# Kernel optimization log

Hardware: AMD Instinct MI355X
Metric: run time of the kernel (lower is better)

## Reference

```python
import jax, jax.numpy as jnp
import numpy as np

EPS = 1e-8
NUM_ITER = 3
NUM_SLOTS = 8
NUM_HEADS = 4


def _ln(x, w, b):
    m = x.mean(-1, keepdims=True)
    v = x.var(-1, keepdims=True)
    return (x - m) / jnp.sqrt(v + 1e-5) * w + b


def setup_inputs() -> dict:
    key = jax.random.key(0)
    B, T, N, D, S, H = 16, 12, 1024, 256, 128, 256
    K = NUM_SLOTS
    ks = jax.random.split(key, 32)
    w = lambda i, shape: (0.02 * jax.random.normal(ks[i], shape)).astype(jnp.float32)
    f32 = jnp.float32
    return {
        'inputs': jax.random.normal(ks[0], (B, T, N, D), f32),
        'slots_noise': jax.random.normal(ks[1], (B, K, S), f32),
        'slot_mu': w(2, (1, 1, S)),
        'slot_log_sigma': w(3, (1, 1, S)),
        'ln_in_w': jnp.ones((D,), f32), 'ln_in_b': jnp.zeros((D,), f32),
        'ln_slots_w': jnp.ones((S,), f32), 'ln_slots_b': jnp.zeros((S,), f32),
        'ln_mlp_w': jnp.ones((S,), f32), 'ln_mlp_b': jnp.zeros((S,), f32),
        'Wq': w(4, (S, S)), 'Wk': w(5, (D, S)), 'Wv': w(6, (D, S)),
        'gru_Wih': w(7, (3 * S, S)), 'gru_Whh': w(8, (3 * S, S)),
        'gru_bih': jnp.zeros((3 * S,), f32), 'gru_bhh': jnp.zeros((3 * S,), f32),
        'mlp_W1': w(9, (S, H)), 'mlp_b1': jnp.zeros((H,), f32),
        'mlp_W2': w(10, (H, S)), 'mlp_b2': jnp.zeros((S,), f32),
        'p_ln1_w': jnp.ones((S,), f32), 'p_ln1_b': jnp.zeros((S,), f32),
        'p_Wq': w(11, (S, S)), 'p_Wk': w(12, (S, S)), 'p_Wv': w(13, (S, S)), 'p_Wo': w(14, (S, S)),
        'p_ln2_w': jnp.ones((S,), f32), 'p_ln2_b': jnp.zeros((S,), f32),
        'p_ffn_W1': w(15, (S, 4 * S)), 'p_ffn_b1': jnp.zeros((4 * S,), f32),
        'p_ffn_W2': w(16, (4 * S, S)), 'p_ffn_b2': jnp.zeros((S,), f32),
        'p_lnf_w': jnp.ones((S,), f32), 'p_lnf_b': jnp.zeros((S,), f32),
    }


def reference(inputs, slots_noise, slot_mu, slot_log_sigma,
              ln_in_w, ln_in_b, ln_slots_w, ln_slots_b, ln_mlp_w, ln_mlp_b,
              Wq, Wk, Wv, gru_Wih, gru_Whh, gru_bih, gru_bhh,
              mlp_W1, mlp_b1, mlp_W2, mlp_b2,
              p_ln1_w, p_ln1_b, p_Wq, p_Wk, p_Wv, p_Wo,
              p_ln2_w, p_ln2_b, p_ffn_W1, p_ffn_b1, p_ffn_W2, p_ffn_b2,
              p_lnf_w, p_lnf_b):
    B, T, N, D = inputs.shape
    S = slot_mu.shape[-1]
    K = NUM_SLOTS

    slots0 = slot_mu + jnp.exp(slot_log_sigma) * slots_noise  # (B,K,S)
    x = _ln(inputs, ln_in_w, ln_in_b)
    k = (x @ Wk) * (S ** -0.5)  # (B,T,N,S), pre-scaled keys
    v = x @ Wv                  # (B,T,N,S)

    def gru(u, h):  # torch GRUCell semantics; u,h: (B*K,S)
        gi = u @ gru_Wih.T + gru_bih
        gh = h @ gru_Whh.T + gru_bhh
        i_r, i_z, i_n = jnp.split(gi, 3, -1)
        h_r, h_z, h_n = jnp.split(gh, 3, -1)
        r = jax.nn.sigmoid(i_r + h_r)
        z = jax.nn.sigmoid(i_z + h_z)
        n = jnp.tanh(i_n + r * h_n)
        return (1.0 - z) * n + z * h

    def mha(y):  # (B,K,S) self-attention, pre-LN block style
        dh = S // NUM_HEADS
        split = lambda t: t.reshape(B, K, NUM_HEADS, dh).transpose(0, 2, 1, 3)
        q = split(y @ p_Wq) * (dh ** -0.5)
        kk = split(y @ p_Wk)
        vv = split(y @ p_Wv)
        a = jax.nn.softmax(jnp.einsum('bhqd,bhkd->bhqk', q, kk), -1)
        o = jnp.einsum('bhqk,bhkd->bhqd', a, vv).transpose(0, 2, 1, 3).reshape(B, K, S)
        return o @ p_Wo

    def predictor(s):
        s = s + mha(_ln(s, p_ln1_w, p_ln1_b))
        h = _ln(s, p_ln2_w, p_ln2_b)
        s = s + (jax.nn.relu(h @ p_ffn_W1 + p_ffn_b1) @ p_ffn_W2 + p_ffn_b2)
        return _ln(s, p_lnf_w, p_lnf_b)

    def step(slots, kv_t):
        k_t, v_t = kv_t  # (B,N,S) each
        attn_vis = None
        for i in range(NUM_ITER):
            slots_prev = slots
            q = _ln(slots, ln_slots_w, ln_slots_b) @ Wq          # (B,K,S)
            logits = jnp.einsum('bns,bks->bnk', k_t, q)           # (B,N,K)
            attn_vis = jax.nn.softmax(logits, -1)                 # over slots
            attn = attn_vis + EPS
            attn = attn / attn.sum(1, keepdims=True)              # normalize over inputs
            updates = jnp.einsum('bnk,bns->bks', attn, v_t)       # (B,K,S)
            slots = gru(updates.reshape(-1, S), slots_prev.reshape(-1, S)).reshape(B, K, S)
            if i < NUM_ITER - 1:
                h = _ln(slots, ln_mlp_w, ln_mlp_b)
                slots = slots + (jax.nn.relu(h @ mlp_W1 + mlp_b1) @ mlp_W2 + mlp_b2)
        return predictor(slots), (slots, attn_vis)

    kT = jnp.swapaxes(k, 0, 1)  # (T,B,N,S)
    vT = jnp.swapaxes(v, 0, 1)
    _, (slots_seq, attn_seq) = jax.lax.scan(step, slots0, (kT, vT))
    slots_collect = jnp.swapaxes(slots_seq, 0, 1)  # (B,T,K,S)
    attns_collect = jnp.swapaxes(attn_seq, 0, 1)   # (B,T,N,K)
    return slots_collect, attns_collect
```

## Files before the change

### kernel.cpp

```cpp
#include <hip/hip_runtime.h>
#include <hip/hip_bf16.h>

typedef _Float16 half8 __attribute__((ext_vector_type(8)));
typedef float floatx4 __attribute__((ext_vector_type(4)));

#define MFMA_F16(a, b, c) __builtin_amdgcn_mfma_f32_16x16x32_f16((a), (b), (c), 0, 0, 0)

struct PrepJobs {
  const float* src[13];
  _Float16* dst[13];
  int In[13], Out[13], elems[13], doT[13];
  float scale[13];
};

__global__ void prep_all_kernel(PrepJobs J) {
  int j = blockIdx.y;
  int idx = blockIdx.x * 256 + threadIdx.x;
  if (idx >= J.elems[j]) return;
  float v;
  if (J.doT[j]) { int o = idx / J.In[j], i = idx - o * J.In[j]; v = J.src[j][i * J.Out[j] + o]; }
  else          { v = J.src[j][idx]; }
  J.dst[j][idx] = (_Float16)(v * J.scale[j]);
}

__global__ void init_ctr_kernel(int* __restrict__ ctr) {
  if (threadIdx.x < 16) ctr[threadIdx.x] = 0;
}

__global__ __launch_bounds__(256) void gemm_kv_kernel(
    const float* __restrict__ x, const float* __restrict__ lnw_g,
    const float* __restrict__ lnb_g, const _Float16* __restrict__ WT,
    _Float16* __restrict__ kout, _Float16* __restrict__ vTout) {
  __shared__ union {
    struct { _Float16 A[128][72]; _Float16 B[128][72]; } s;
    _Float16 C[128][136];
  } u;
  __shared__ float s_mean[128], s_rstd[128], s_red[256][2], s_lnw[256], s_lnb[256];

  const int tid = threadIdx.x;
  const int bx = blockIdx.x, y = blockIdx.y;
  const size_t r0 = (size_t)bx * 128;
  const int w = tid >> 6, lane = tid & 63, quad = lane >> 4, l15 = lane & 15;

  s_lnw[tid] = lnw_g[tid];
  s_lnb[tid] = lnb_g[tid];
  {
    int row = tid >> 1, half = tid & 1;
    const float* p = x + (r0 + row) * 256 + half * 128;
    float s = 0.f, sq = 0.f;
    for (int i = 0; i < 32; i++) {
      float4 d = ((const float4*)p)[i];
      s += d.x + d.y + d.z + d.w;
      sq += d.x * d.x + d.y * d.y + d.z * d.z + d.w * d.w;
    }
    s_red[tid][0] = s; s_red[tid][1] = sq;
  }
  __syncthreads();
  if (tid < 128) {
    float s  = s_red[2 * tid][0] + s_red[2 * tid + 1][0];
    float sq = s_red[2 * tid][1] + s_red[2 * tid + 1][1];
    float m = s * (1.f / 256.f);
    float v = sq * (1.f / 256.f) - m * m;
    s_mean[tid] = m; s_rstd[tid] = rsqrtf(v + 1e-5f);
  }

  floatx4 acc[2][8];
  for (int rt = 0; rt < 2; rt++)
    for (int ct = 0; ct < 8; ct++) acc[rt][ct] = (floatx4){0.f, 0.f, 0.f, 0.f};

  for (int c = 0; c < 4; c++) {
    __syncthreads();
    for (int i = 0; i < 4; i++) {
      int g = tid + 256 * i;
      int row = g >> 3, c8 = g & 7;
      int col0 = c * 64 + c8 * 8;
      const float* p = x + (r0 + row) * 256 + col0;
      float4 d0 = ((const float4*)p)[0];
      float4 d1 = ((const float4*)p)[1];
      float f[8] = {d0.x, d0.y, d0.z, d0.w, d1.x, d1.y, d1.z, d1.w};
      float m = s_mean[row], rs = s_rstd[row];
      half8 hv;
      #pragma unroll
      for (int j = 0; j < 8; j++)
        hv[j] = (_Float16)((f[j] - m) * rs * s_lnw[col0 + j] + s_lnb[col0 + j]);
      *(half8*)&u.s.A[row][c8 * 8] = hv;
      *(half8*)&u.s.B[row][c8 * 8] = *(const half8*)(WT + (size_t)(y * 128 + row) * 256 + col0);
    }
    __syncthreads();
    #pragma unroll
    for (int ks = 0; ks < 2; ks++) {
      half8 af[2];
      af[0] = *(const half8*)&u.s.A[(2 * w) * 16 + l15][ks * 32 + quad * 8];
      af[1] = *(const half8*)&u.s.A[(2 * w + 1) * 16 + l15][ks * 32 + quad * 8];
      #pragma unroll
      for (int ct = 0; ct < 8; ct++) {
        half8 bf = *(const half8*)&u.s.B[ct * 16 + l15][ks * 32 + quad * 8];
        acc[0][ct] = MFMA_F16(af[0], bf, acc[0][ct]);
        acc[1][ct] = MFMA_F16(af[1], bf, acc[1][ct]);
      }
    }
  }

  const size_t bt = (size_t)(bx >> 3);
  const int n0loc = (bx & 7) * 128;
  if (y == 0) {
    for (int rt = 0; rt < 2; rt++)
      for (int ct = 0; ct < 8; ct++)
        #pragma unroll
        for (int r = 0; r < 4; r++) {
          size_t row = r0 + (2 * w + rt) * 16 + quad * 4 + r;
          kout[row * 128 + ct * 16 + l15] = (_Float16)acc[rt][ct][r];
        }
  } else {
    __syncthreads();
    for (int rt = 0; rt < 2; rt++)
      for (int ct = 0; ct < 8; ct++)
        #pragma unroll
        for (int r = 0; r < 4; r++)
          u.C[(2 * w + rt) * 16 + quad * 4 + r][ct * 16 + l15] = (_Float16)acc[rt][ct][r];
    __syncthreads();
    int s = tid >> 1, hf = tid & 1;
    for (int j = 0; j < 8; j++) {
      int nb = hf * 64 + j * 8;
      half8 tmp;
      #pragma unroll
      for (int e = 0; e < 8; e++) tmp[e] = u.C[nb + e][s];
      *(half8*)(vTout + (bt * 128 + s) * 1024 + n0loc + nb) = tmp;
    }
  }
}

struct P2Args {
  const _Float16 *kbuf, *vT;
  const _Float16 *WqT, *Wih, *Whh, *W1T, *W2T;
  const _Float16 *pQT, *pKT, *pVT, *pOT, *pF1T, *pF2T;
  const float *noise, *mu, *lsig;
  const float *lnsw, *lnsb, *lnmw, *lnmb;
  const float *bih, *bhh, *mb1, *mb2;
  const float *pl1w, *pl1b, *pl2w, *pl2b, *fb1, *fb2, *plfw, *plfb;
  float *out_slots, *out_attn;
  float *upd_p;
  float *col_p;
  float *vs_p;
  int   *ctr;
};

struct SH {
  _Float16 k_lds[128][136];
  _Float16 v_lds[128][136];
  float slots[8][128];
  _Float16 a16[16][136];
  _Float16 h16[16][136];
  float gi[8][384];
  float gh[8][384];
  union {
    struct { _Float16 qT[16][136]; _Float16 attnT[16][136]; } sa;
    struct { _Float16 m16[16][264]; } mlp;
    struct { float qh[8][128]; float kh[8][128]; float vh[8][128]; float sc[4][8][8]; } mha;
    struct { _Float16 f16[16][520]; } ffn;
  } u;
  float colsum[8];
  float vsum[128];
  float bih[384], bhh[384], mb1[256], mb2[128], fb1[512], fb2[128];
  float lnsw[128], lnsb[128], lnmw[128], lnmb[128];
  float pl1w[128], pl1b[128], pl2w[128], pl2b[128], plfw[128], plfb[128];
};

__device__ __forceinline__ void group_barrier(int* ctr, int target) {
  __syncthreads();
  if (threadIdx.x == 0) {
    __hip_atomic_fetch_add(ctr, 1, __ATOMIC_ACQ_REL, __HIP_MEMORY_SCOPE_AGENT);
    while (__hip_atomic_load(ctr, __ATOMIC_ACQUIRE, __HIP_MEMORY_SCOPE_AGENT) < target)
      __builtin_amdgcn_s_sleep(1);
  }
  __syncthreads();
}

__device__ __forceinline__ void ln_to_a16(SH* sh, const float (*src)[128],
                                          const float* wv, const float* bv,
                                          int w, int lane) {
  if (w < 8) {
    float x0 = src[w][lane], x1 = src[w][lane + 64];
    float s = x0 + x1, sq = x0 * x0 + x1 * x1;
    #pragma unroll
    for (int m = 1; m < 64; m <<= 1) { s += __shfl_xor(s, m); sq += __shfl_xor(sq, m); }
    float mn = s * 0.0078125f;
    float vr = sq * 0.0078125f - mn * mn;
    float rs = rsqrtf(vr + 1e-5f);
    sh->a16[w][lane]      = (_Float16)((x0 - mn) * rs * wv[lane]      + bv[lane]);
    sh->a16[w][lane + 64] = (_Float16)((x1 - mn) * rs * wv[lane + 64] + bv[lane + 64]);
  } else {
    sh->a16[w][lane] = (_Float16)0.f;
    sh->a16[w][lane + 64] = (_Float16)0.f;
  }
}

__global__ __launch_bounds__(1024, 4) void slot_attn_kernel(P2Args P) {
  __shared__ SH sh;
  const int tid = threadIdx.x;
  const int w = tid >> 6, lane = tid & 63, quad = lane >> 4, l15 = lane & 15;
  const int b = blockIdx.x & 15;
  const int g = blockIdx.x >> 4;
  const int n0 = g * 128;
  int* ctrb = P.ctr + b;
  int bar_phase = 0;

  for (int i = tid; i < 384; i += 1024) { sh.bih[i] = P.bih[i]; sh.bhh[i] = P.bhh[i]; }
  for (int i = tid; i < 256; i += 1024) sh.mb1[i] = P.mb1[i];
  for (int i = tid; i < 512; i += 1024) sh.fb1[i] = P.fb1[i];
  if (tid < 128) {
    sh.mb2[tid]  = P.mb2[tid];  sh.fb2[tid]  = P.fb2[tid];
    sh.lnsw[tid] = P.lnsw[tid]; sh.lnsb[tid] = P.lnsb[tid];
    sh.lnmw[tid] = P.lnmw[tid]; sh.lnmb[tid] = P.lnmb[tid];
    sh.pl1w[tid] = P.pl1w[tid]; sh.pl1b[tid] = P.pl1b[tid];
    sh.pl2w[tid] = P.pl2w[tid]; sh.pl2b[tid] = P.pl2b[tid];
    sh.plfw[tid] = P.plfw[tid]; sh.plfb[tid] = P.plfb[tid];
  }
  {
    int kk = tid >> 7, s = tid & 127;
    sh.slots[kk][s] = P.mu[s] + expf(P.lsig[s]) * P.noise[(b * 8 + kk) * 128 + s];
  }
  __syncthreads();

  for (int t = 0; t < 12; t++) {
    const _Float16* kt = P.kbuf + ((size_t)(b * 12 + t)) * 1024 * 128 + (size_t)n0 * 128;
    const _Float16* vt = P.vT   + ((size_t)(b * 12 + t)) * 128 * 1024 + n0;
    {
      int r = tid >> 4, c8 = (tid & 15) * 8;
      #pragma unroll
      for (int p = 0; p < 2; p++) {
        int row = p * 64 + r;
        *(half8*)&sh.k_lds[row][c8] = *(const half8*)(kt + (size_t)row * 128 + c8);
        *(half8*)&sh.v_lds[row][c8] = *(const half8*)(vt + (size_t)row * 1024 + c8);
      }
    }
    if (tid < 128) sh.vsum[tid] = 0.f;
    __syncthreads();
    {
      int s = tid >> 3, j = tid & 7;
      float a = 0.f;
      #pragma unroll
      for (int e = 0; e < 16; e++) a += (float)sh.v_lds[s][j * 16 + e];
      atomicAdd(&sh.vsum[s], a);
    }
    __syncthreads();
    if (tid < 128)
      __hip_atomic_store(&P.vs_p[(b * 8 + g) * 128 + tid], sh.vsum[tid],
                         __ATOMIC_RELAXED, __HIP_MEMORY_SCOPE_AGENT);

    for (int it = 0; it < 3; it++) {
      const int par = (t * 3 + it) & 1;
      float* updg = P.upd_p + ((size_t)(par * 16 + b) * 8 + g) * 1024;
      float* colg = P.col_p + ((size_t)(par * 16 + b) * 8 + g) * 8;
      if (w < 8) {
        float x0 = sh.slots[w][lane], x1 = sh.slots[w][lane + 64];
        sh.h16[w][lane] = (_Float16)x0; sh.h16[w][lane + 64] = (_Float16)x1;
        float s = x0 + x1, sq = x0 * x0 + x1 * x1;
        #pragma unroll
        for (int m = 1; m < 64; m <<= 1) { s += __shfl_xor(s, m); sq += __shfl_xor(sq, m); }
        float mn = s * 0.0078125f;
        float vr = sq * 0.0078125f - mn * mn;
        float rs = rsqrtf(vr + 1e-5f);
        sh.a16[w][lane]      = (_Float16)((x0 - mn) * rs * sh.lnsw[lane]      + sh.lnsb[lane]);
        sh.a16[w][lane + 64] = (_Float16)((x1 - mn) * rs * sh.lnsw[lane + 64] + sh.lnsb[lane + 64]);
      } else {
        sh.h16[w][lane] = (_Float16)0.f; sh.h16[w][lane + 64] = (_Float16)0.f;
        sh.a16[w][lane] = (_Float16)0.f; sh.a16[w][lane + 64] = (_Float16)0.f;
      }
      if (tid < 8) sh.colsum[tid] = 0.f;
      __syncthreads();
      if (w < 8) {
        floatx4 acc = (floatx4){0.f, 0.f, 0.f, 0.f};
        const _Float16* ar = &sh.a16[l15][quad * 8];
        const _Float16* br = P.WqT + (size_t)(w * 16 + l15) * 128 + quad * 8;
        #pragma unroll
        for (int ks = 0; ks < 4; ks++)
          acc = MFMA_F16(*(const half8*)(ar + ks * 32), *(const half8*)(br + ks * 32), acc);
        #pragma unroll
        for (int r = 0; r < 4; r++)
          sh.u.sa.qT[quad * 4 + r][w * 16 + l15] = (_Float16)acc[r];
      } else {
        const int idx8 = w - 8;
        const _Float16* ar = &sh.h16[l15][quad * 8];
        #pragma unroll
        for (int tt = 0; tt < 2; tt++) {
          int ct = idx8 + tt * 8;
          const _Float16* Bg = P.Whh + (size_t)(ct * 16 + l15) * 128 + quad * 8;
          floatx4 acc = (floatx4){0.f, 0.f, 0.f, 0.f};
          #pragma unroll
          for (int ks = 0; ks < 4; ks++)
            acc = MFMA_F16(*(const half8*)(ar + ks * 32), *(const half8*)(Bg + ks * 32), acc);
          int col = ct * 16 + l15;
          #pragma unroll
          for (int r = 0; r < 4; r++) {
            int slot = quad * 4 + r;
            if (slot < 8) sh.gh[slot][col] = acc[r] + sh.bhh[col];
          }
        }
      }
      __syncthreads();
      if (w < 8) {
        int nloc0 = w * 16;
        floatx4 acc = (floatx4){0.f, 0.f, 0.f, 0.f};
        const _Float16* ar = &sh.k_lds[nloc0 + l15][quad * 8];
        const _Float16* br = &sh.u.sa.qT[l15][quad * 8];
        #pragma unroll
        for (int ks = 0; ks < 4; ks++)
          acc = MFMA_F16(*(const half8*)(ar + ks * 32), *(const half8*)(br + ks * 32), acc);
        float cs = 0.f;
        #pragma unroll
        for (int r = 0; r < 4; r++) {
          float v = (l15 < 8) ? acc[r] : -3.0e38f;
          float mx = v;
          mx = fmaxf(mx, __shfl_xor(mx, 1, 16));
          mx = fmaxf(mx, __shfl_xor(mx, 2, 16));
          mx = fmaxf(mx, __shfl_xor(mx, 4, 16));
          mx = fmaxf(mx, __shfl_xor(mx, 8, 16));
          float pv = (l15 < 8) ? expf(v - mx) : 0.f;
          float ss = pv;
          ss += __shfl_xor(ss, 1, 16); ss += __shfl_xor(ss, 2, 16);
          ss += __shfl_xor(ss, 4, 16); ss += __shfl_xor(ss, 8, 16);
          float pn = pv / ss;
          cs += pn;
          int nloc = nloc0 + quad * 4 + r;
          sh.u.sa.attnT[l15][nloc] = (_Float16)pn;
          if (it == 2 && l15 < 8)
            P.out_attn[((size_t)(b * 12 + t) * 1024 + n0 + nloc) * 8 + l15] = pn;
        }
        cs += __shfl_xor(cs, 16); cs += __shfl_xor(cs, 32);
        if (lane < 8) atomicAdd(&sh.colsum[lane], cs);
      } else {
        const int idx8 = w - 8;
        int ct = idx8 + 16;
        const _Float16* ar = &sh.h16[l15][quad * 8];
        const _Float16* Bg = P.Whh + (size_t)(ct * 16 + l15) * 128 + quad * 8;
        floatx4 acc = (floatx4){0.f, 0.f, 0.f, 0.f};
        #pragma unroll
        for (int ks = 0; ks < 4; ks++)
          acc = MFMA_F16(*(const half8*)(ar + ks * 32), *(const half8*)(Bg + ks * 32), acc);
        int col = ct * 16 + l15;
        #pragma unroll
        for (int r = 0; r < 4; r++) {
          int slot = quad * 4 + r;
          if (slot < 8) sh.gh[slot][col] = acc[r] + sh.bhh[col];
        }
      }
      __syncthreads();
      if (w < 8) {
        floatx4 acc = (floatx4){0.f, 0.f, 0.f, 0.f};
        const _Float16* ar = &sh.u.sa.attnT[l15][quad * 8];
        const _Float16* br = &sh.v_lds[w * 16 + l15][quad * 8];
        #pragma unroll
        for (int ks = 0; ks < 4; ks++)
          acc = MFMA_F16(*(const half8*)(ar + ks * 32), *(const half8*)(br + ks * 32), acc);
        int scol = w * 16 + l15;
        #pragma unroll
        for (int r = 0; r < 4; r++) {
          int slot = quad * 4 + r;
          if (slot < 8)
            __hip_atomic_store(&updg[slot * 128 + scol], acc[r],
                               __ATOMIC_RELAXED, __HIP_MEMORY_SCOPE_AGENT);
        }
      }
      if (tid < 8)
        __hip_atomic_store(&colg[tid], sh.colsum[tid],
                           __ATOMIC_RELAXED, __HIP_MEMORY_SCOPE_AGENT);
      bar_phase++;
      group_barrier(ctrb, 8 * bar_phase);
      {
        int slot = tid >> 7, scol = tid & 127;
        const float* up = P.upd_p + (size_t)(par * 16 + b) * 8 * 1024 + slot * 128 + scol;
        float sum = 0.f;
        #pragma unroll
        for (int gg = 0; gg < 8; gg++)
          sum += __hip_atomic_load((float*)(up + gg * 1024),
                                   __ATOMIC_RELAXED, __HIP_MEMORY_SCOPE_AGENT);
        float csum = 0.f;
        if (tid < 8) {
          const float* cp = P.col_p + (size_t)(par * 16 + b) * 8 * 8 + tid;
          #pragma unroll
          for (int gg = 0; gg < 8; gg++)
            csum += __hip_atomic_load((float*)(cp + gg * 8),
                                      __ATOMIC_RELAXED, __HIP_MEMORY_SCOPE_AGENT);
        }
        float vtot = 0.f;
        if (it == 0 && tid < 128) {
          const float* vp = P.vs_p + b * 8 * 128 + tid;
          #pragma unroll
          for (int gg = 0; gg < 8; gg++)
            vtot += __hip_atomic_load((float*)(vp + gg * 128),
                                      __ATOMIC_RELAXED, __HIP_MEMORY_SCOPE_AGENT);
        }
        __syncthreads();
        if (tid < 8) sh.colsum[tid] = csum;
        if (it == 0 && tid < 128) sh.vsum[tid] = vtot;
        __syncthreads();
        float upd = (sum + 1e-8f * sh.vsum[scol]) / (sh.colsum[slot] + 1024.f * 1e-8f);
        sh.a16[slot][scol] = (_Float16)upd;
      }
      __syncthreads();
      {
        const _Float16* ar = &sh.a16[l15][quad * 8];
        const _Float16* Bg = P.Wih + (size_t)(w * 16 + l15) * 128 + quad * 8;
        floatx4 acc = (floatx4){0.f, 0.f, 0.f, 0.f};
        #pragma unroll
        for (int ks = 0; ks < 4; ks++)
          acc = MFMA_F16(*(const half8*)(ar + ks * 32), *(const half8*)(Bg + ks * 32), acc);
        int col = w * 16 + l15;
        #pragma unroll
        for (int r = 0; r < 4; r++) {
          int slot = quad * 4 + r;
          if (slot < 8) sh.gi[slot][col] = acc[r] + sh.bih[col];
        }
        if (w < 8) {
          int col2 = (16 + w) * 16 + l15;
          const _Float16* Bg2 = P.Wih + (size_t)((16 + w) * 16 + l15) * 128 + quad * 8;
          floatx4 acc2 = (floatx4){0.f, 0.f, 0.f, 0.f};
          #pragma unroll
          for (int ks = 0; ks < 4; ks++)
            acc2 = MFMA_F16(*(const half8*)(ar + ks * 32), *(const half8*)(Bg2 + ks * 32), acc2);
          #pragma unroll
          for (int r = 0; r < 4; r++) {
            int slot = quad * 4 + r;
            if (slot < 8) sh.gi[slot][col2] = acc2[r] + sh.bih[col2];
          }
        }
      }
      __syncthreads();
      if (w < 8) {
        float h0 = sh.slots[w][lane], h1 = sh.slots[w][lane + 64];
        float r0 = 1.f / (1.f + expf(-(sh.gi[w][lane]       + sh.gh[w][lane])));
        float z0 = 1.f / (1.f + expf(-(sh.gi[w][128 + lane] + sh.gh[w][128 + lane])));
        float n0v = tanhf(sh.gi[w][256 + lane] + r0 * sh.gh[w][256 + lane]);
        float x0 = (1.f - z0) * n0v + z0 * h0;
        int l64 = lane + 64;
        float r1 = 1.f / (1.f + expf(-(sh.gi[w][l64]       + sh.gh[w][l64])));
        float z1 = 1.f / (1.f + expf(-(sh.gi[w][128 + l64] + sh.gh[w][128 + l64])));
        float n1v = tanhf(sh.gi[w][256 + l64] + r1 * sh.gh[w][256 + l64]);
        float x1 = (1.f - z1) * n1v + z1 * h1;
        sh.slots[w][lane] = x0; sh.slots[w][lane + 64] = x1;
        if (it == 2 && g == 0) {
          P.out_slots[((size_t)(b * 12 + t) * 8 + w) * 128 + lane]      = x0;
          P.out_slots[((size_t)(b * 12 + t) * 8 + w) * 128 + lane + 64] = x1;
        }
        const float* wv = (it < 2) ? sh.lnmw : sh.pl1w;
        const float* bv = (it < 2) ? sh.lnmb : sh.pl1b;
        float s = x0 + x1, sq = x0 * x0 + x1 * x1;
        #pragma unroll
        for (int m = 1; m < 64; m <<= 1) { s += __shfl_xor(s, m); sq += __shfl_xor(sq, m); }
        float mn = s * 0.0078125f;
        float vr = sq * 0.0078125f - mn * mn;
        float rs = rsqrtf(vr + 1e-5f);
        sh.a16[w][lane]      = (_Float16)((x0 - mn) * rs * wv[lane]      + bv[lane]);
        sh.a16[w][lane + 64] = (_Float16)((x1 - mn) * rs * wv[lane + 64] + bv[lane + 64]);
      }
      __syncthreads();
      if (it < 2) {
        {
          floatx4 acc = (floatx4){0.f, 0.f, 0.f, 0.f};
          const _Float16* ar = &sh.a16[l15][quad * 8];
          const _Float16* br = P.W1T + (size_t)(w * 16 + l15) * 128 + quad * 8;
          #pragma unroll
          for (int ks = 0; ks < 4; ks++)
            acc = MFMA_F16(*(const half8*)(ar + ks * 32), *(const half8*)(br + ks * 32), acc);
          int col = w * 16 + l15;
          #pragma unroll
          for (int r = 0; r < 4; r++) {
            int slot = quad * 4 + r;
            if (slot < 8) sh.u.mlp.m16[slot][col] = (_Float16)fmaxf(acc[r] + sh.mb1[col], 0.f);
            else          sh.u.mlp.m16[slot][col] = (_Float16)0.f;
          }
        }
        __syncthreads();
        if (w < 8) {
          floatx4 acc = (floatx4){0.f, 0.f, 0.f, 0.f};
          const _Float16* ar = &sh.u.mlp.m16[l15][quad * 8];
          const _Float16* br = P.W2T + (size_t)(w * 16 + l15) * 256 + quad * 8;
          #pragma unroll
          for (int ks = 0; ks < 8; ks++)
            acc = MFMA_F16(*(const half8*)(ar + ks * 32), *(const half8*)(br + ks * 32), acc);
          int col = w * 16 + l15;
          #pragma unroll
          for (int r = 0; r < 4; r++) {
            int slot = quad * 4 + r;
            if (slot < 8) sh.slots[slot][col] += acc[r] + sh.mb2[col];
          }
        }
        __syncthreads();
      }
    }

    {
      const _Float16* ar = &sh.a16[l15][quad * 8];
      int gg = w >> 3, ct = w & 7, col = ct * 16 + l15;
      const _Float16* Bg = (gg == 0 ? P.pQT : P.pKT) + (size_t)(ct * 16 + l15) * 128 + quad * 8;
      floatx4 acc = (floatx4){0.f, 0.f, 0.f, 0.f};
      #pragma unroll
      for (int ks = 0; ks < 4; ks++)
        acc = MFMA_F16(*(const half8*)(ar + ks * 32), *(const half8*)(Bg + ks * 32), acc);
      float scale = (gg == 0) ? 0.17677669529663687f : 1.f;
      float* dst = (gg == 0) ? &sh.u.mha.qh[0][0] : &sh.u.mha.kh[0][0];
      #pragma unroll
      for (int r = 0; r < 4; r++) {
        int slot = quad * 4 + r;
        if (slot < 8) dst[slot * 128 + col] = acc[r] * scale;
      }
      if (w < 8) {
        const _Float16* Bg2 = P.pVT + (size_t)(w * 16 + l15) * 128 + quad * 8;
        floatx4 a2 = (floatx4){0.f, 0.f, 0.f, 0.f};
        #pragma unroll
        for (int ks = 0; ks < 4; ks++)
          a2 = MFMA_F16(*(const half8*)(ar + ks * 32), *(const half8*)(Bg2 + ks * 32), a2);
        int colv = w * 16 + l15;
        #pragma unroll
        for (int r = 0; r < 4; r++) {
          int slot = quad * 4 + r;
          if (slot < 8) sh.u.mha.vh[slot][colv] = a2[r];
        }
      }
    }
    __syncthreads();
    if (tid < 256) {
      int h = tid >> 6, a = (tid >> 3) & 7, b2 = tid & 7;
      const float* qr = &sh.u.mha.qh[a][h * 32];
      const float* kr = &sh.u.mha.kh[b2][h * 32];
      float s = 0.f;
      #pragma unroll
      for (int d = 0; d < 32; d++) s += qr[d] * kr[d];
      sh.u.mha.sc[h][a][b2] = s;
    }
    __syncthreads();
    if (tid < 32) {
      int h = tid >> 3, a = tid & 7;
      float* p = sh.u.mha.sc[h][a];
      float mx = p[0];
      #pragma unroll
      for (int j = 1; j < 8; j++) mx = fmaxf(mx, p[j]);
      float e[8]; float ssum = 0.f;
      #pragma unroll
      for (int j = 0; j < 8; j++) { e[j] = expf(p[j] - mx); ssum += e[j]; }
      float inv = 1.f / ssum;
      #pragma unroll
      for (int j = 0; j < 8; j++) p[j] = e[j] * inv;
    }
    __syncthreads();
    {
      int a = tid >> 7, col = tid & 127, h = col >> 5;
      float acc = 0.f;
      #pragma unroll
      for (int b2 = 0; b2 < 8; b2++) acc += sh.u.mha.sc[h][a][b2] * sh.u.mha.vh[b2][col];
      sh.a16[a][col] = (_Float16)acc;
    }
    __syncthreads();
    if (w < 8) {
      floatx4 acc = (floatx4){0.f, 0.f, 0.f, 0.f};
      const _Float16* ar = &sh.a16[l15][quad * 8];
      const _Float16* br = P.pOT + (size_t)(w * 16 + l15) * 128 + quad * 8;
      #pragma unroll
      for (int ks = 0; ks < 4; ks++)
        acc = MFMA_F16(*(const half8*)(ar + ks * 32), *(const half8*)(br + ks * 32), acc);
      int col = w * 16 + l15;
      #pragma unroll
      for (int r = 0; r < 4; r++) {
        int slot = quad * 4 + r;
        if (slot < 8) sh.slots[slot][col] += acc[r];
      }
    }
    __syncthreads();
    ln_to_a16(&sh, sh.slots, sh.pl2w, sh.pl2b, w, lane);
    __syncthreads();
    for (int ct = w; ct < 32; ct += 16) {
      floatx4 acc = (floatx4){0.f, 0.f, 0.f, 0.f};
      const _Float16* ar = &sh.a16[l15][quad * 8];
      const _Float16* br = P.pF1T + (size_t)(ct * 16 + l15) * 128 + quad * 8;
      #pragma unroll
      for (int ks = 0; ks < 4; ks++)
        acc = MFMA_F16(*(const half8*)(ar + ks * 32), *(const half8*)(br + ks * 32), acc);
      int col = ct * 16 + l15;
      #pragma unroll
      for (int r = 0; r < 4; r++) {
        int slot = quad * 4 + r;
        if (slot < 8) sh.u.ffn.f16[slot][col] = (_Float16)fmaxf(acc[r] + sh.fb1[col], 0.f);
        else          sh.u.ffn.f16[slot][col] = (_Float16)0.f;
      }
    }
    __syncthreads();
    if (w < 8) {
      floatx4 acc = (floatx4){0.f, 0.f, 0.f, 0.f};
      const _Float16* ar = &sh.u.ffn.f16[l15][quad * 8];
      const _Float16* br = P.pF2T + (size_t)(w * 16 + l15) * 512 + quad * 8;
      #pragma unroll 4
      for (int ks = 0; ks < 16; ks++)
        acc = MFMA_F16(*(const half8*)(ar + ks * 32), *(const half8*)(br + ks * 32), acc);
      int col = w * 16 + l15;
      #pragma unroll
      for (int r = 0; r < 4; r++) {
        int slot = quad * 4 + r;
        if (slot < 8) sh.slots[slot][col] += acc[r] + sh.fb2[col];
      }
    }
    __syncthreads();
    if (w < 8) {
      float x0 = sh.slots[w][lane], x1 = sh.slots[w][lane + 64];
      float s = x0 + x1, sq = x0 * x0 + x1 * x1;
      #pragma unroll
      for (int m = 1; m < 64; m <<= 1) { s += __shfl_xor(s, m); sq += __shfl_xor(sq, m); }
      float mn = s * 0.0078125f;
      float vr = sq * 0.0078125f - mn * mn;
      float rs = rsqrtf(vr + 1e-5f);
      sh.slots[w][lane]      = (x0 - mn) * rs * sh.plfw[lane]      + sh.plfb[lane];
      sh.slots[w][lane + 64] = (x1 - mn) * rs * sh.plfw[lane + 64] + sh.plfb[lane + 64];
    }
    __syncthreads();
  }
}

extern "C" void kernel_launch(void* const* d_in, const int* in_sizes, int n_in,
                              void* d_out, int out_size, void* d_ws, size_t ws_size,
                              hipStream_t stream) {
  const float* inp   = (const float*)d_in[0];
  const float* noise = (const float*)d_in[1];
  const float* mu    = (const float*)d_in[2];
  const float* lsig  = (const float*)d_in[3];
  const float* lniw  = (const float*)d_in[4];
  const float* lnib  = (const float*)d_in[5];
  const float* lnsw  = (const float*)d_in[6];
  const float* lnsb  = (const float*)d_in[7];
  const float* lnmw  = (const float*)d_in[8];
  const float* lnmb  = (const float*)d_in[9];
  const float* Wq    = (const float*)d_in[10];
  const float* Wk    = (const float*)d_in[11];
  const float* Wv    = (const float*)d_in[12];
  const float* gWih  = (const float*)d_in[13];
  const float* gWhh  = (const float*)d_in[14];
  const float* gbih  = (const float*)d_in[15];
  const float* gbhh  = (const float*)d_in[16];
  const float* mW1   = (const float*)d_in[17];
  const float* mb1   = (const float*)d_in[18];
  const float* mW2   = (const float*)d_in[19];
  const float* mb2   = (const float*)d_in[20];
  const float* pl1w  = (const float*)d_in[21];
  const float* pl1b  = (const float*)d_in[22];
  const float* pWq   = (const float*)d_in[23];
  const float* pWk   = (const float*)d_in[24];
  const float* pWv   = (const float*)d_in[25];
  const float* pWo   = (const float*)d_in[26];
  const float* pl2w  = (const float*)d_in[27];
  const float* pl2b  = (const float*)d_in[28];
  const float* pf1   = (const float*)d_in[29];
  const float* pfb1  = (const float*)d_in[30];
  const float* pf2   = (const float*)d_in[31];
  const float* pfb2  = (const float*)d_in[32];
  const float* plfw  = (const float*)d_in[33];
  const float* plfb  = (const float*)d_in[34];

  _Float16* p   = (_Float16*)d_ws;
  _Float16* kbuf = p;  p += 25165824;
  _Float16* vT   = p;  p += 25165824;
  _Float16* WT   = p;  p += 65536;
  _Float16* WqT  = p;  p += 16384;
  _Float16* Wih  = p;  p += 49152;
  _Float16* Whh  = p;  p += 49152;
  _Float16* W1T  = p;  p += 32768;
  _Float16* W2T  = p;  p += 32768;
  _Float16* pQT  = p;  p += 16384;
  _Float16* pKT  = p;  p += 16384;
  _Float16* pVT  = p;  p += 16384;
  _Float16* pOT  = p;  p += 16384;
  _Float16* pF1T = p;  p += 65536;
  _Float16* pF2T = p;  p += 65536;
  float* fb   = (float*)p;
  float* upd_p = fb;  fb += 2 * 16 * 8 * 1024;
  float* col_p = fb;  fb += 2 * 16 * 8 * 8;
  float* vs_p  = fb;  fb += 16 * 8 * 128;
  int*   ctr   = (int*)fb;

  const float kscale = 0.08838834764831845f;
  init_ctr_kernel<<<1, 64, 0, stream>>>(ctr);

  PrepJobs J;
  const float* srcs[13] = {Wk, Wv, Wq, gWih, gWhh, mW1, mW2, pWq, pWk, pWv, pWo, pf1, pf2};
  _Float16* dsts[13]    = {WT, WT + 32768, WqT, Wih, Whh, W1T, W2T, pQT, pKT, pVT, pOT, pF1T, pF2T};
  int Ins[13]    = {256, 256, 128, 49152, 49152, 128, 256, 128, 128, 128, 128, 128, 512};
  int Outs[13]   = {128, 128, 128, 1, 1, 256, 128, 128, 128, 128, 128, 512, 128};
  int elemss[13] = {32768, 32768, 16384, 49152, 49152, 32768, 32768, 16384, 16384, 16384, 16384, 65536, 65536};
  int doTs[13]   = {1, 1, 1, 0, 0, 1, 1, 1, 1, 1, 1, 1, 1};
  float scales[13] = {kscale, 1.f, 1.f, 1.f, 1.f, 1.f, 1.f, 1.f, 1.f, 1.f, 1.f, 1.f, 1.f};
  for (int j = 0; j < 13; j++) {
    J.src[j] = srcs[j]; J.dst[j] = dsts[j]; J.In[j] = Ins[j]; J.Out[j] = Outs[j];
    J.elems[j] = elemss[j]; J.doT[j] = doTs[j]; J.scale[j] = scales[j];
  }
  dim3 gp(256, 13, 1);
  prep_all_kernel<<<gp, 256, 0, stream>>>(J);

  dim3 g1(1536, 2, 1);
  gemm_kv_kernel<<<g1, 256, 0, stream>>>(inp, lniw, lnib, WT, kbuf, vT);

  P2Args a;
  a.kbuf = kbuf; a.vT = vT;
  a.WqT = WqT; a.Wih = Wih; a.Whh = Whh; a.W1T = W1T; a.W2T = W2T;
  a.pQT = pQT; a.pKT = pKT; a.pVT = pVT; a.pOT = pOT; a.pF1T = pF1T; a.pF2T = pF2T;
  a.noise = noise; a.mu = mu; a.lsig = lsig;
  a.lnsw = lnsw; a.lnsb = lnsb; a.lnmw = lnmw; a.lnmb = lnmb;
  a.bih = gbih; a.bhh = gbhh; a.mb1 = mb1; a.mb2 = mb2;
  a.pl1w = pl1w; a.pl1b = pl1b; a.pl2w = pl2w; a.pl2b = pl2b;
  a.fb1 = pfb1; a.fb2 = pfb2; a.plfw = plfw; a.plfb = plfb;
  a.out_slots = (float*)d_out;
  a.out_attn  = (float*)d_out + 196608;
  a.upd_p = upd_p; a.col_p = col_p; a.vs_p = vs_p; a.ctr = ctr;

  slot_attn_kernel<<<128, 1024, 0, stream>>>(a);
}
```

Baseline: 1.355 ms.

## Fold Wq into K projection and trim barriers in slot-attention loop

Precomputes W̃ = Wk·Wqᵀ (scaled) so the key buffer already holds k·Wqᵀ. The iteration loop can then use the layer-normed slots directly as the query, which removes the per-iteration Wq MFMA and one block barrier. The Whh GEMM tiles are redistributed across the freed phases. Counters and column partials are padded to 64-element strides, likely to avoid false sharing. The cross-block reduction drops a sync pair by having each thread load the column sums itself, and the predictor MHA softmax and AV product are fused into one shuffle-based phase, removing two barriers. The risk is fp16 rounding of the folded weight, which changes numerics slightly.

```diff
diff --git a/kernel.cpp b/kernel.cpp
--- a/kernel.cpp
+++ b/kernel.cpp
@@ -7,10 +7,10 @@
 #define MFMA_F16(a, b, c) __builtin_amdgcn_mfma_f32_16x16x32_f16((a), (b), (c), 0, 0, 0)
 
 struct PrepJobs {
-  const float* src[13];
-  _Float16* dst[13];
-  int In[13], Out[13], elems[13], doT[13];
-  float scale[13];
+  const float* src[11];
+  _Float16* dst[11];
+  int In[11], Out[11], elems[11], doT[11];
+  float scale[11];
 };
 
 __global__ void prep_all_kernel(PrepJobs J) {
@@ -23,8 +23,20 @@
   J.dst[j][idx] = (_Float16)(v * J.scale[j]);
 }
 
+__global__ void prep_wtilde_kernel(const float* __restrict__ Wk, const float* __restrict__ Wq,
+                                   _Float16* __restrict__ WT, float scale) {
+  int idx = blockIdx.x * 256 + threadIdx.x;
+  int s = idx >> 8, i = idx & 255;
+  const float* wk = Wk + (size_t)i * 128;
+  const float* wq = Wq + (size_t)s * 128;
+  float acc = 0.f;
+  #pragma unroll 4
+  for (int o = 0; o < 128; o++) acc += wk[o] * wq[o];
+  WT[idx] = (_Float16)(acc * scale);
+}
+
 __global__ void init_ctr_kernel(int* __restrict__ ctr) {
-  if (threadIdx.x < 16) ctr[threadIdx.x] = 0;
+  ctr[threadIdx.x] = 0;
 }
 
 __global__ __launch_bounds__(256) void gemm_kv_kernel(
@@ -132,7 +144,7 @@
 
 struct P2Args {
   const _Float16 *kbuf, *vT;
-  const _Float16 *WqT, *Wih, *Whh, *W1T, *W2T;
+  const _Float16 *Wih, *Whh, *W1T, *W2T;
   const _Float16 *pQT, *pKT, *pVT, *pOT, *pF1T, *pF2T;
   const float *noise, *mu, *lsig;
   const float *lnsw, *lnsb, *lnmw, *lnmb;
@@ -202,7 +214,7 @@
   const int b = blockIdx.x & 15;
   const int g = blockIdx.x >> 4;
   const int n0 = g * 128;
-  int* ctrb = P.ctr + b;
+  int* ctrb = P.ctr + b * 64;
   int bar_phase = 0;
 
   for (int i = tid; i < 384; i += 1024) { sh.bih[i] = P.bih[i]; sh.bhh[i] = P.bhh[i]; }
@@ -251,7 +263,7 @@
     for (int it = 0; it < 3; it++) {
       const int par = (t * 3 + it) & 1;
       float* updg = P.upd_p + ((size_t)(par * 16 + b) * 8 + g) * 1024;
-      float* colg = P.col_p + ((size_t)(par * 16 + b) * 8 + g) * 8;
+      float* colg = P.col_p + ((size_t)(par * 16 + b) * 8 + g) * 64;
       if (w < 8) {
         float x0 = sh.slots[w][lane], x1 = sh.slots[w][lane + 64];
         sh.h16[w][lane] = (_Float16)x0; sh.h16[w][lane + 64] = (_Float16)x1;
@@ -270,40 +282,10 @@
       if (tid < 8) sh.colsum[tid] = 0.f;
       __syncthreads();
       if (w < 8) {
-        floatx4 acc = (floatx4){0.f, 0.f, 0.f, 0.f};
-        const _Float16* ar = &sh.a16[l15][quad * 8];
-        const _Float16* br = P.WqT + (size_t)(w * 16 + l15) * 128 + quad * 8;
-        #pragma unroll
-        for (int ks = 0; ks < 4; ks++)
-          acc = MFMA_F16(*(const half8*)(ar + ks * 32), *(const half8*)(br + ks * 32), acc);
-        #pragma unroll
-        for (int r = 0; r < 4; r++)
-          sh.u.sa.qT[quad * 4 + r][w * 16 + l15] = (_Float16)acc[r];
-      } else {
-        const int idx8 = w - 8;
-        const _Float16* ar = &sh.h16[l15][quad * 8];
-        #pragma unroll
-        for (int tt = 0; tt < 2; tt++) {
-          int ct = idx8 + tt * 8;
-          const _Float16* Bg = P.Whh + (size_t)(ct * 16 + l15) * 128 + quad * 8;
-          floatx4 acc = (floatx4){0.f, 0.f, 0.f, 0.f};
-          #pragma unroll
-          for (int ks = 0; ks < 4; ks++)
-            acc = MFMA_F16(*(const half8*)(ar + ks * 32), *(const half8*)(Bg + ks * 32), acc);
-          int col = ct * 16 + l15;
-          #pragma unroll
-          for (int r = 0; r < 4; r++) {
-            int slot = quad * 4 + r;
-            if (slot < 8) sh.gh[slot][col] = acc[r] + sh.bhh[col];
-          }
-        }
-      }
-      __syncthreads();
-      if (w < 8) {
         int nloc0 = w * 16;
         floatx4 acc = (floatx4){0.f, 0.f, 0.f, 0.f};
         const _Float16* ar = &sh.k_lds[nloc0 + l15][quad * 8];
-        const _Float16* br = &sh.u.sa.qT[l15][quad * 8];
+        const _Float16* br = &sh.a16[l15][quad * 8];
         #pragma unroll
         for (int ks = 0; ks < 4; ks++)
           acc = MFMA_F16(*(const half8*)(ar + ks * 32), *(const half8*)(br + ks * 32), acc);
@@ -331,18 +313,21 @@
         if (lane < 8) atomicAdd(&sh.colsum[lane], cs);
       } else {
         const int idx8 = w - 8;
-        int ct = idx8 + 16;
         const _Float16* ar = &sh.h16[l15][quad * 8];
-        const _Float16* Bg = P.Whh + (size_t)(ct * 16 + l15) * 128 + quad * 8;
-        floatx4 acc = (floatx4){0.f, 0.f, 0.f, 0.f};
-        #pragma unroll
-        for (int ks = 0; ks < 4; ks++)
-          acc = MFMA_F16(*(const half8*)(ar + ks * 32), *(const half8*)(Bg + ks * 32), acc);
-        int col = ct * 16 + l15;
-        #pragma unroll
-        for (int r = 0; r < 4; r++) {
-          int slot = quad * 4 + r;
-          if (slot < 8) sh.gh[slot][col] = acc[r] + sh.bhh[col];
+        #pragma unroll
+        for (int tt = 0; tt < 2; tt++) {
+          int ct = idx8 + tt * 8;
+          const _Float16* Bg = P.Whh + (size_t)(ct * 16 + l15) * 128 + quad * 8;
+          floatx4 acc = (floatx4){0.f, 0.f, 0.f, 0.f};
+          #pragma unroll
+          for (int ks = 0; ks < 4; ks++)
+            acc = MFMA_F16(*(const half8*)(ar + ks * 32), *(const half8*)(Bg + ks * 32), acc);
+          int col = ct * 16 + l15;
+          #pragma unroll
+          for (int r = 0; r < 4; r++) {
+            int slot = quad * 4 + r;
+            if (slot < 8) sh.gh[slot][col] = acc[r] + sh.bhh[col];
+          }
         }
       }
       __syncthreads();
@@ -360,6 +345,21 @@
           if (slot < 8)
             __hip_atomic_store(&updg[slot * 128 + scol], acc[r],
                                __ATOMIC_RELAXED, __HIP_MEMORY_SCOPE_AGENT);
+        }
+      } else {
+        const int idx8 = w - 8;
+        int ct = idx8 + 16;
+        const _Float16* ar = &sh.h16[l15][quad * 8];
+        const _Float16* Bg = P.Whh + (size_t)(ct * 16 + l15) * 128 + quad * 8;
+        floatx4 acc = (floatx4){0.f, 0.f, 0.f, 0.f};
+        #pragma unroll
+        for (int ks = 0; ks < 4; ks++)
+          acc = MFMA_F16(*(const half8*)(ar + ks * 32), *(const half8*)(Bg + ks * 32), acc);
+        int col = ct * 16 + l15;
+        #pragma unroll
+        for (int r = 0; r < 4; r++) {
+          int slot = quad * 4 + r;
+          if (slot < 8) sh.gh[slot][col] = acc[r] + sh.bhh[col];
         }
       }
       if (tid < 8)
@@ -375,27 +375,26 @@
         for (int gg = 0; gg < 8; gg++)
           sum += __hip_atomic_load((float*)(up + gg * 1024),
                                    __ATOMIC_RELAXED, __HIP_MEMORY_SCOPE_AGENT);
+        const float* cp = P.col_p + (size_t)(par * 16 + b) * 8 * 64 + slot;
         float csum = 0.f;
-        if (tid < 8) {
-          const float* cp = P.col_p + (size_t)(par * 16 + b) * 8 * 8 + tid;
-          #pragma unroll
-          for (int gg = 0; gg < 8; gg++)
-            csum += __hip_atomic_load((float*)(cp + gg * 8),
-                                      __ATOMIC_RELAXED, __HIP_MEMORY_SCOPE_AGENT);
-        }
-        float vtot = 0.f;
-        if (it == 0 && tid < 128) {
-          const float* vp = P.vs_p + b * 8 * 128 + tid;
+        #pragma unroll
+        for (int gg = 0; gg < 8; gg++)
+          csum += __hip_atomic_load((float*)(cp + gg * 64),
+                                    __ATOMIC_RELAXED, __HIP_MEMORY_SCOPE_AGENT);
+        float vsv;
+        if (it == 0) {
+          const float* vp = P.vs_p + b * 8 * 128 + scol;
+          float vtot = 0.f;
           #pragma unroll
           for (int gg = 0; gg < 8; gg++)
             vtot += __hip_atomic_load((float*)(vp + gg * 128),
                                       __ATOMIC_RELAXED, __HIP_MEMORY_SCOPE_AGENT);
-        }
-        __syncthreads();
-        if (tid < 8) sh.colsum[tid] = csum;
-        if (it == 0 && tid < 128) sh.vsum[tid] = vtot;
-        __syncthreads();
-        float upd = (sum + 1e-8f * sh.vsum[scol]) / (sh.colsum[slot] + 1024.f * 1e-8f);
+          if (slot == 0) sh.vsum[scol] = vtot;
+          vsv = vtot;
+        } else {
+          vsv = sh.vsum[scol];
+        }
+        float upd = (sum + 1e-8f * vsv) / (csum + 1024.f * 1e-8f);
         sh.a16[slot][scol] = (_Float16)upd;
       }
       __syncthreads();
@@ -520,36 +519,33 @@
       }
     }
     __syncthreads();
-    if (tid < 256) {
-      int h = tid >> 6, a = (tid >> 3) & 7, b2 = tid & 7;
+    if (w < 4) {
+      int h = w, a = lane >> 3, b2 = lane & 7;
       const float* qr = &sh.u.mha.qh[a][h * 32];
       const float* kr = &sh.u.mha.kh[b2][h * 32];
       float s = 0.f;
       #pragma unroll
       for (int d = 0; d < 32; d++) s += qr[d] * kr[d];
-      sh.u.mha.sc[h][a][b2] = s;
-    }
-    __syncthreads();
-    if (tid < 32) {
-      int h = tid >> 3, a = tid & 7;
-      float* p = sh.u.mha.sc[h][a];
-      float mx = p[0];
-      #pragma unroll
-      for (int j = 1; j < 8; j++) mx = fmaxf(mx, p[j]);
-      float e[8]; float ssum = 0.f;
-      #pragma unroll
-      for (int j = 0; j < 8; j++) { e[j] = expf(p[j] - mx); ssum += e[j]; }
-      float inv = 1.f / ssum;
-      #pragma unroll
-      for (int j = 0; j < 8; j++) p[j] = e[j] * inv;
-    }
-    __syncthreads();
-    {
-      int a = tid >> 7, col = tid & 127, h = col >> 5;
-      float acc = 0.f;
-      #pragma unroll
-      for (int b2 = 0; b2 < 8; b2++) acc += sh.u.mha.sc[h][a][b2] * sh.u.mha.vh[b2][col];
-      sh.a16[a][col] = (_Float16)acc;
+      float mx = s;
+      mx = fmaxf(mx, __shfl_xor(mx, 1, 8));
+      mx = fmaxf(mx, __shfl_xor(mx, 2, 8));
+      mx = fmaxf(mx, __shfl_xor(mx, 4, 8));
+      float e = expf(s - mx);
+      float ssum = e;
+      ssum += __shfl_xor(ssum, 1, 8); ssum += __shfl_xor(ssum, 2, 8); ssum += __shfl_xor(ssum, 4, 8);
+      float p = e / ssum;
+      float o0 = 0.f, o1 = 0.f, o2 = 0.f, o3 = 0.f;
+      int d0 = h * 32 + b2 * 4;
+      #pragma unroll
+      for (int j = 0; j < 8; j++) {
+        float pj = __shfl(p, (a << 3) + j);
+        const float* vr = &sh.u.mha.vh[j][d0];
+        o0 += pj * vr[0]; o1 += pj * vr[1]; o2 += pj * vr[2]; o3 += pj * vr[3];
+      }
+      sh.a16[a][d0]     = (_Float16)o0;
+      sh.a16[a][d0 + 1] = (_Float16)o1;
+      sh.a16[a][d0 + 2] = (_Float16)o2;
+      sh.a16[a][d0 + 3] = (_Float16)o3;
     }
     __syncthreads();
     if (w < 8) {
@@ -671,34 +667,36 @@
   _Float16* pF2T = p;  p += 65536;
   float* fb   = (float*)p;
   float* upd_p = fb;  fb += 2 * 16 * 8 * 1024;
-  float* col_p = fb;  fb += 2 * 16 * 8 * 8;
+  float* col_p = fb;  fb += 2 * 16 * 8 * 64;
   float* vs_p  = fb;  fb += 16 * 8 * 128;
   int*   ctr   = (int*)fb;
+  (void)WqT;
 
   const float kscale = 0.08838834764831845f;
-  init_ctr_kernel<<<1, 64, 0, stream>>>(ctr);
+  init_ctr_kernel<<<1, 1024, 0, stream>>>(ctr);
 
   PrepJobs J;
-  const float* srcs[13] = {Wk, Wv, Wq, gWih, gWhh, mW1, mW2, pWq, pWk, pWv, pWo, pf1, pf2};
-  _Float16* dsts[13]    = {WT, WT + 32768, WqT, Wih, Whh, W1T, W2T, pQT, pKT, pVT, pOT, pF1T, pF2T};
-  int Ins[13]    = {256, 256, 128, 49152, 49152, 128, 256, 128, 128, 128, 128, 128, 512};
-  int Outs[13]   = {128, 128, 128, 1, 1, 256, 128, 128, 128, 128, 128, 512, 128};
-  int elemss[13] = {32768, 32768, 16384, 49152, 49152, 32768, 32768, 16384, 16384, 16384, 16384, 65536, 65536};
-  int doTs[13]   = {1, 1, 1, 0, 0, 1, 1, 1, 1, 1, 1, 1, 1};
-  float scales[13] = {kscale, 1.f, 1.f, 1.f, 1.f, 1.f, 1.f, 1.f, 1.f, 1.f, 1.f, 1.f, 1.f};
-  for (int j = 0; j < 13; j++) {
+  const float* srcs[11] = {Wv, gWih, gWhh, mW1, mW2, pWq, pWk, pWv, pWo, pf1, pf2};
+  _Float16* dsts[11]    = {WT + 32768, Wih, Whh, W1T, W2T, pQT, pKT, pVT, pOT, pF1T, pF2T};
+  int Ins[11]    = {256, 49152, 49152, 128, 256, 128, 128, 128, 128, 128, 512};
+  int Outs[11]   = {128, 1, 1, 256, 128, 128, 128, 128, 128, 512, 128};
+  int elemss[11] = {32768, 49152, 49152, 32768, 32768, 16384, 16384, 16384, 16384, 65536, 65536};
+  int doTs[11]   = {1, 0, 0, 1, 1, 1, 1, 1, 1, 1, 1};
+  float scales[11] = {1.f, 1.f, 1.f, 1.f, 1.f, 1.f, 1.f, 1.f, 1.f, 1.f, 1.f};
+  for (int j = 0; j < 11; j++) {
     J.src[j] = srcs[j]; J.dst[j] = dsts[j]; J.In[j] = Ins[j]; J.Out[j] = Outs[j];
     J.elems[j] = elemss[j]; J.doT[j] = doTs[j]; J.scale[j] = scales[j];
   }
-  dim3 gp(256, 13, 1);
+  dim3 gp(256, 11, 1);
   prep_all_kernel<<<gp, 256, 0, stream>>>(J);
+  prep_wtilde_kernel<<<128, 256, 0, stream>>>(Wk, Wq, WT, kscale);
 
   dim3 g1(1536, 2, 1);
   gemm_kv_kernel<<<g1, 256, 0, stream>>>(inp, lniw, lnib, WT, kbuf, vT);
 
   P2Args a;
   a.kbuf = kbuf; a.vT = vT;
-  a.WqT = WqT; a.Wih = Wih; a.Whh = Whh; a.W1T = W1T; a.W2T = W2T;
+  a.Wih = Wih; a.Whh = Whh; a.W1T = W1T; a.W2T = W2T;
   a.pQT = pQT; a.pKT = pKT; a.pVT = pVT; a.pOT = pOT; a.pF1T = pF1T; a.pF2T = pF2T;
   a.noise = noise; a.mu = mu; a.lsig = lsig;
   a.lnsw = lnsw; a.lnsb = lnsb; a.lnmw = lnmw; a.lnmb = lnmb;
```

Result: faster. 1.244 ms (-8.2%).
